# Optimization experiments

Hardware: AMD Instinct MI355X
Metric: run time of the kernel (lower is better)

The kernel has to match this reference:

```python
import jax, jax.numpy as jnp
import numpy as np

D_MODEL = 512
SEQ_LEN = 2048
S = 32  # local window size
BATCH = 2


def setup_inputs() -> dict:
    key = jax.random.key(0)
    ks = jax.random.split(key, 12)
    shp = (SEQ_LEN, BATCH, D_MODEL)
    return {
        "query": jax.random.normal(ks[0], shp, jnp.float32),
        "key": jax.random.normal(ks[1], shp, jnp.float32),
        "value": jax.random.normal(ks[2], shp, jnp.float32),
        "Wq": jax.random.normal(ks[3], (D_MODEL, D_MODEL), jnp.float32) * 0.02,
        "bq": jax.random.normal(ks[4], (D_MODEL,), jnp.float32) * 0.01,
        "Wk": jax.random.normal(ks[5], (D_MODEL, D_MODEL), jnp.float32) * 0.02,
        "bk": jax.random.normal(ks[6], (D_MODEL,), jnp.float32) * 0.01,
        "Wv": jax.random.normal(ks[7], (D_MODEL, D_MODEL), jnp.float32) * 0.02,
        "bv": jax.random.normal(ks[8], (D_MODEL,), jnp.float32) * 0.01,
        "pos_bias": jax.random.normal(ks[9], (SEQ_LEN, SEQ_LEN), jnp.float32) * 0.02,
        "Wo": jax.random.normal(ks[10], (D_MODEL, D_MODEL), jnp.float32) * 0.02,
        "bo": jax.random.normal(ks[11], (D_MODEL,), jnp.float32) * 0.01,
    }


def _aft_local(query, key, value, Wq, bq, Wk, bk, Wv, bv, pos_bias, Wo, bo):
    T, B, D = query.shape
    q = query @ Wq.T + bq  # [T,B,D]
    k = key @ Wk.T + bk
    v = value @ Wv.T + bv
    pb = pos_bias[:T, :T]

    # max_logit: elementwise max of per-dim key max and (key + col-max of pos_bias) max,
    # then batch index 0 (faithful to original `[0]` indexing) -> shape [D]
    max_logit = jnp.maximum(k.max(axis=0),
                            (k + pb.max(axis=0)[:, None, None]).max(axis=0))[0]

    # out-of-window running sums: tokens t' <= t - S contribute exp(k) (no pos bias)
    ek = jnp.exp(k - max_logit)                 # [T,B,D]
    cs_num = jnp.cumsum(ek * v, axis=0)
    cs_den = jnp.cumsum(ek, axis=0)
    t_arr = jnp.arange(T)
    prefix_idx = jnp.clip(t_arr - S, 0, T - 1)
    has_prefix = (t_arr >= S)[:, None, None]
    num_out = jnp.where(has_prefix, cs_num[prefix_idx], 0.0)
    den_out = jnp.where(has_prefix, cs_den[prefix_idx], 0.0)

    # in-window part: t' in [max(0, t-S+1), t] with pos_bias[t, t']
    j = jnp.arange(S)
    idx_raw = t_arr[:, None] - S + 1 + j[None, :]   # [T,S]
    valid = (idx_raw >= 0).astype(k.dtype)
    idx = jnp.clip(idx_raw, 0, T - 1)
    k_win = k[idx]                                  # [T,S,B,D]
    v_win = v[idx]                                  # [T,S,B,D]
    pb_win = pb[t_arr[:, None], idx]                # [T,S]
    exp_l = jnp.exp(k_win + pb_win[:, :, None, None] - max_logit) * valid[:, :, None, None]
    num_in = (exp_l * v_win).sum(axis=1)            # [T,B,D]
    den_in = exp_l.sum(axis=1)

    y = jax.nn.sigmoid(q) * (num_out + num_in) / (den_out + den_in)
    return y @ Wo.T + bo


def reference(query, key, value, Wq, bq, Wk, bk, Wv, bv, pos_bias, Wo, bo):
    return _aft_local(query, key, value, Wq, bq, Wk, bk, Wv, bv, pos_bias, Wo, bo)
```

## Files before the change

### kernel.cpp

```cpp
#include <hip/hip_runtime.h>
#include <hip/hip_bf16.h>

#define TT 2048
#define BB 2
#define DD 512
#define BD (BB*DD)
#define SS 32
#define MR (TT*BB)
#define NE (TT*BB*DD)
#define CH 32

typedef __bf16 bf16x8 __attribute__((ext_vector_type(8)));
typedef float f32x4 __attribute__((ext_vector_type(4)));

__device__ __forceinline__ void async_copy16(void* lds, const void* gptr) {
    __builtin_amdgcn_global_load_lds(
        (const __attribute__((address_space(1))) void*)gptr,
        (__attribute__((address_space(3))) void*)lds,
        16, 0, 0);
}

__global__ __launch_bounds__(256) void cast_all(
    const float* __restrict__ s0, const float* __restrict__ s1, const float* __restrict__ s2,
    const float* __restrict__ w0, const float* __restrict__ w1,
    const float* __restrict__ w2, const float* __restrict__ w3,
    __hip_bfloat16* __restrict__ d0, __hip_bfloat16* __restrict__ d1, __hip_bfloat16* __restrict__ d2,
    __hip_bfloat16* __restrict__ e0, __hip_bfloat16* __restrict__ e1,
    __hip_bfloat16* __restrict__ e2, __hip_bfloat16* __restrict__ e3)
{
    int b = blockIdx.x;
    const float* s;
    __hip_bfloat16* d;
    size_t i;
    if (b < 6144) {
        int which = b >> 11;
        s = which == 0 ? s0 : (which == 1 ? s1 : s2);
        d = which == 0 ? d0 : (which == 1 ? d1 : d2);
        i = ((size_t)(b & 2047) * 256 + threadIdx.x) * 4;
    } else {
        int b2 = b - 6144;
        int which = b2 >> 8;
        s = which == 0 ? w0 : (which == 1 ? w1 : (which == 2 ? w2 : w3));
        d = which == 0 ? e0 : (which == 1 ? e1 : (which == 2 ? e2 : e3));
        i = ((size_t)(b2 & 255) * 256 + threadIdx.x) * 4;
    }
    float4 f = *(const float4*)(s + i);
    union { __hip_bfloat16 h[4]; ushort4 u; } cv;
    cv.h[0] = __float2bfloat16(f.x); cv.h[1] = __float2bfloat16(f.y);
    cv.h[2] = __float2bfloat16(f.z); cv.h[3] = __float2bfloat16(f.w);
    *(ushort4*)((unsigned short*)d + i) = cv.u;
}

__global__ __launch_bounds__(256) void gemm_qkv(
    const __hip_bfloat16* __restrict__ qb, const __hip_bfloat16* __restrict__ kb,
    const __hip_bfloat16* __restrict__ vb,
    const __hip_bfloat16* __restrict__ Wqb, const __hip_bfloat16* __restrict__ Wkb,
    const __hip_bfloat16* __restrict__ Wvb,
    const float* __restrict__ bq, const float* __restrict__ bk,
    const float* __restrict__ bv,
    float* __restrict__ qout, float* __restrict__ ek, float* __restrict__ ekv,
    float* __restrict__ part_d, float* __restrict__ part_n)
{
    __shared__ char smem[16384];
    const int tid = threadIdx.x;
    const int lane = tid & 63;
    const int wv = tid >> 6;
    const int wave_m = wv >> 1, wave_n = wv & 1;
    const int m0 = blockIdx.y * 64, n0 = blockIdx.x * 64;
    const int kq = lane >> 4, rr = lane & 15;

    if (blockIdx.z == 0) {
        f32x4 acc[2][2] = {};
        const __hip_bfloat16* Arow = qb + (size_t)(m0 + lane) * DD + wv * 8;
        const __hip_bfloat16* Wrow = Wqb + (size_t)(n0 + lane) * DD + wv * 8;
        char* ldsA = &smem[wv * 1024];
        char* ldsW = &smem[4096 + wv * 1024];
        for (int k0 = 0; k0 < DD; k0 += 32) {
            __syncthreads();
            async_copy16(ldsA, Arow + k0);
            async_copy16(ldsW, Wrow + k0);
            __syncthreads();
            bf16x8 a0 = *(const bf16x8*)&smem[kq*1024 + (wave_m*32 +  0 + rr)*16];
            bf16x8 a1 = *(const bf16x8*)&smem[kq*1024 + (wave_m*32 + 16 + rr)*16];
            bf16x8 b0 = *(const bf16x8*)&smem[4096 + kq*1024 + (wave_n*32 +  0 + rr)*16];
            bf16x8 b1 = *(const bf16x8*)&smem[4096 + kq*1024 + (wave_n*32 + 16 + rr)*16];
            acc[0][0] = __builtin_amdgcn_mfma_f32_16x16x32_bf16(a0, b0, acc[0][0], 0, 0, 0);
            acc[0][1] = __builtin_amdgcn_mfma_f32_16x16x32_bf16(a0, b1, acc[0][1], 0, 0, 0);
            acc[1][0] = __builtin_amdgcn_mfma_f32_16x16x32_bf16(a1, b0, acc[1][0], 0, 0, 0);
            acc[1][1] = __builtin_amdgcn_mfma_f32_16x16x32_bf16(a1, b1, acc[1][1], 0, 0, 0);
        }
        #pragma unroll
        for (int ms = 0; ms < 2; ++ms)
            #pragma unroll
            for (int ns = 0; ns < 2; ++ns) {
                int n = n0 + wave_n*32 + ns*16 + rr;
                float bn = bq[n];
                #pragma unroll
                for (int r = 0; r < 4; ++r) {
                    int m = m0 + wave_m*32 + ms*16 + kq*4 + r;
                    qout[(size_t)m * DD + n] = acc[ms][ns][r] + bn;
                }
            }
    } else {
        f32x4 acck[2][2] = {}, accv[2][2] = {};
        const __hip_bfloat16* AKrow = kb + (size_t)(m0 + lane) * DD + wv * 8;
        const __hip_bfloat16* WKrow = Wkb + (size_t)(n0 + lane) * DD + wv * 8;
        const __hip_bfloat16* AVrow = vb + (size_t)(m0 + lane) * DD + wv * 8;
        const __hip_bfloat16* WVrow = Wvb + (size_t)(n0 + lane) * DD + wv * 8;
        char* ldsAK = &smem[wv * 1024];
        char* ldsWK = &smem[4096 + wv * 1024];
        char* ldsAV = &smem[8192 + wv * 1024];
        char* ldsWV = &smem[12288 + wv * 1024];
        for (int k0 = 0; k0 < DD; k0 += 32) {
            __syncthreads();
            async_copy16(ldsAK, AKrow + k0);
            async_copy16(ldsWK, WKrow + k0);
            async_copy16(ldsAV, AVrow + k0);
            async_copy16(ldsWV, WVrow + k0);
            __syncthreads();
            bf16x8 ak0 = *(const bf16x8*)&smem[kq*1024 + (wave_m*32 +  0 + rr)*16];
            bf16x8 ak1 = *(const bf16x8*)&smem[kq*1024 + (wave_m*32 + 16 + rr)*16];
            bf16x8 bk0 = *(const bf16x8*)&smem[4096 + kq*1024 + (wave_n*32 +  0 + rr)*16];
            bf16x8 bk1 = *(const bf16x8*)&smem[4096 + kq*1024 + (wave_n*32 + 16 + rr)*16];
            bf16x8 av0 = *(const bf16x8*)&smem[8192 + kq*1024 + (wave_m*32 +  0 + rr)*16];
            bf16x8 av1 = *(const bf16x8*)&smem[8192 + kq*1024 + (wave_m*32 + 16 + rr)*16];
            bf16x8 bv0 = *(const bf16x8*)&smem[12288 + kq*1024 + (wave_n*32 +  0 + rr)*16];
            bf16x8 bv1 = *(const bf16x8*)&smem[12288 + kq*1024 + (wave_n*32 + 16 + rr)*16];
            acck[0][0] = __builtin_amdgcn_mfma_f32_16x16x32_bf16(ak0, bk0, acck[0][0], 0, 0, 0);
            acck[0][1] = __builtin_amdgcn_mfma_f32_16x16x32_bf16(ak0, bk1, acck[0][1], 0, 0, 0);
            acck[1][0] = __builtin_amdgcn_mfma_f32_16x16x32_bf16(ak1, bk0, acck[1][0], 0, 0, 0);
            acck[1][1] = __builtin_amdgcn_mfma_f32_16x16x32_bf16(ak1, bk1, acck[1][1], 0, 0, 0);
            accv[0][0] = __builtin_amdgcn_mfma_f32_16x16x32_bf16(av0, bv0, accv[0][0], 0, 0, 0);
            accv[0][1] = __builtin_amdgcn_mfma_f32_16x16x32_bf16(av0, bv1, accv[0][1], 0, 0, 0);
            accv[1][0] = __builtin_amdgcn_mfma_f32_16x16x32_bf16(av1, bv0, accv[1][0], 0, 0, 0);
            accv[1][1] = __builtin_amdgcn_mfma_f32_16x16x32_bf16(av1, bv1, accv[1][1], 0, 0, 0);
        }
        float sd[2][2] = {{0.f,0.f},{0.f,0.f}};
        float sn[2][2] = {{0.f,0.f},{0.f,0.f}};
        #pragma unroll
        for (int ms = 0; ms < 2; ++ms)
            #pragma unroll
            for (int ns = 0; ns < 2; ++ns) {
                int n = n0 + wave_n*32 + ns*16 + rr;
                float bkn = bk[n], bvn = bv[n];
                #pragma unroll
                for (int r = 0; r < 4; ++r) {
                    int m = m0 + wave_m*32 + ms*16 + kq*4 + r;
                    float e  = expf(acck[ms][ns][r] + bkn);
                    float nv = e * (accv[ms][ns][r] + bvn);
                    ek[(size_t)m * DD + n]  = e;
                    ekv[(size_t)m * DD + n] = nv;
                    sd[ns][r & 1] += e;
                    sn[ns][r & 1] += nv;
                }
            }
        #pragma unroll
        for (int ns = 0; ns < 2; ++ns)
            #pragma unroll
            for (int par = 0; par < 2; ++par) {
                sd[ns][par] += __shfl_xor(sd[ns][par], 16, 64);
                sd[ns][par] += __shfl_xor(sd[ns][par], 32, 64);
                sn[ns][par] += __shfl_xor(sn[ns][par], 16, 64);
                sn[ns][par] += __shfl_xor(sn[ns][par], 32, 64);
            }
        __syncthreads();
        float* red = (float*)smem;
        if (lane < 16) {
            #pragma unroll
            for (int ns = 0; ns < 2; ++ns) {
                int c = wave_n*32 + ns*16 + rr;
                red[(0*2 + wave_m)*64 + c] = sd[ns][0];
                red[(1*2 + wave_m)*64 + c] = sd[ns][1];
                red[(2*2 + wave_m)*64 + c] = sn[ns][0];
                red[(3*2 + wave_m)*64 + c] = sn[ns][1];
            }
        }
        __syncthreads();
        {
            int which = tid >> 6;
            int c = tid & 63;
            float s = red[(which*2 + 0)*64 + c] + red[(which*2 + 1)*64 + c];
            int b = which & 1;
            float* dst = (which < 2) ? part_d : part_n;
            dst[(size_t)blockIdx.y * BD + b*512 + n0 + c] = s;
        }
    }
}

__global__ __launch_bounds__(256) void fused_window(
    const float* __restrict__ q, const float* __restrict__ ek,
    const float* __restrict__ ekv, const float* __restrict__ part_d,
    const float* __restrict__ part_n, const float* __restrict__ pb,
    __hip_bfloat16* __restrict__ yb)
{
    __shared__ float wl[CH][SS];
    const int tid = threadIdx.x;
    const int col = blockIdx.x * 256 + tid;
    const int chunk = blockIdx.y;
    const int t0 = chunk * CH;

    #pragma unroll
    for (int i = 0; i < (CH * SS) / 256; ++i) {
        int idx = tid + i * 256;
        int tl = idx >> 5, j = idx & 31;
        int t = t0 + tl;
        int u = t - (SS - 1) + j;
        float w = 0.f;
        if (u >= 0) w = expf(pb[(size_t)t * TT + u]);
        wl[tl][j] = w;
    }
    __syncthreads();

    float ring_d[32], ring_n[32];
    float cs_d = 0.f, cs_n = 0.f;
    const bool hasp = (chunk > 0);
    if (hasp) {
        float pref_d = 0.f, pref_n = 0.f;
        for (int p = 0; p < chunk; ++p) {
            pref_d += part_d[(size_t)p * BD + col];
            pref_n += part_n[(size_t)p * BD + col];
        }
        float ssd = 0.f, ssn = 0.f;
        #pragma unroll
        for (int i = 0; i < 32; ++i) {
            size_t off = (size_t)(t0 - 32 + i) * BD + col;
            float e = ek[off];
            float n = ekv[off];
            ring_d[i] = e; ring_n[i] = n;
            ssd += e; ssn += n;
        }
        cs_d = pref_d - ssd;
        cs_n = pref_n - ssn;
    } else {
        #pragma unroll
        for (int i = 0; i < 32; ++i) { ring_d[i] = 0.f; ring_n[i] = 0.f; }
    }

    #pragma unroll
    for (int s = 0; s < CH; ++s) {
        int t = t0 + s;
        size_t off = (size_t)t * BD + col;
        float e = ek[off];
        float n = ekv[off];
        cs_d += ring_d[s];
        cs_n += ring_n[s];
        ring_d[s] = e;
        ring_n[s] = n;
        float den = 0.f, num = 0.f;
        #pragma unroll
        for (int j4 = 0; j4 < 8; ++j4) {
            float4 w4 = *(const float4*)&wl[s][j4 * 4];
            den += w4.x * ring_d[(s + 1 + j4*4 + 0) & 31];
            num += w4.x * ring_n[(s + 1 + j4*4 + 0) & 31];
            den += w4.y * ring_d[(s + 1 + j4*4 + 1) & 31];
            num += w4.y * ring_n[(s + 1 + j4*4 + 1) & 31];
            den += w4.z * ring_d[(s + 1 + j4*4 + 2) & 31];
            num += w4.z * ring_n[(s + 1 + j4*4 + 2) & 31];
            den += w4.w * ring_d[(s + 1 + j4*4 + 3) & 31];
            num += w4.w * ring_n[(s + 1 + j4*4 + 3) & 31];
        }
        if (hasp) { den += cs_d; num += cs_n; }
        float qv = q[off];
        float sig = 1.f / (1.f + expf(-qv));
        yb[off] = __float2bfloat16(sig * num / den);
    }
}

__global__ __launch_bounds__(256) void gemm_out(
    const __hip_bfloat16* __restrict__ yb, const __hip_bfloat16* __restrict__ Wob,
    const float* __restrict__ bo, float* __restrict__ out)
{
    __shared__ char smem[8192];
    const int tid = threadIdx.x;
    const int lane = tid & 63;
    const int wv = tid >> 6;
    const int wave_m = wv >> 1, wave_n = wv & 1;
    const int m0 = blockIdx.y * 64, n0 = blockIdx.x * 64;
    const int kq = lane >> 4, rr = lane & 15;

    f32x4 acc[2][2] = {};
    const __hip_bfloat16* Arow = yb + (size_t)(m0 + lane) * DD + wv * 8;
    const __hip_bfloat16* Wrow = Wob + (size_t)(n0 + lane) * DD + wv * 8;
    char* ldsA = &smem[wv * 1024];
    char* ldsW = &smem[4096 + wv * 1024];

    for (int k0 = 0; k0 < DD; k0 += 32) {
        __syncthreads();
        async_copy16(ldsA, Arow + k0);
        async_copy16(ldsW, Wrow + k0);
        __syncthreads();
        bf16x8 a0 = *(const bf16x8*)&smem[kq*1024 + (wave_m*32 +  0 + rr)*16];
        bf16x8 a1 = *(const bf16x8*)&smem[kq*1024 + (wave_m*32 + 16 + rr)*16];
        bf16x8 b0 = *(const bf16x8*)&smem[4096 + kq*1024 + (wave_n*32 +  0 + rr)*16];
        bf16x8 b1 = *(const bf16x8*)&smem[4096 + kq*1024 + (wave_n*32 + 16 + rr)*16];
        acc[0][0] = __builtin_amdgcn_mfma_f32_16x16x32_bf16(a0, b0, acc[0][0], 0, 0, 0);
        acc[0][1] = __builtin_amdgcn_mfma_f32_16x16x32_bf16(a0, b1, acc[0][1], 0, 0, 0);
        acc[1][0] = __builtin_amdgcn_mfma_f32_16x16x32_bf16(a1, b0, acc[1][0], 0, 0, 0);
        acc[1][1] = __builtin_amdgcn_mfma_f32_16x16x32_bf16(a1, b1, acc[1][1], 0, 0, 0);
    }
    #pragma unroll
    for (int ms = 0; ms < 2; ++ms)
        #pragma unroll
        for (int ns = 0; ns < 2; ++ns) {
            int n = n0 + wave_n*32 + ns*16 + rr;
            float bn = bo[n];
            #pragma unroll
            for (int r = 0; r < 4; ++r) {
                int m = m0 + wave_m*32 + ms*16 + kq*4 + r;
                out[(size_t)m * DD + n] = acc[ms][ns][r] + bn;
            }
        }
}

extern "C" void kernel_launch(void* const* d_in, const int* in_sizes, int n_in,
                              void* d_out, int out_size, void* d_ws, size_t ws_size,
                              hipStream_t stream) {
    const float* query = (const float*)d_in[0];
    const float* key   = (const float*)d_in[1];
    const float* value = (const float*)d_in[2];
    const float* Wq    = (const float*)d_in[3];
    const float* bq    = (const float*)d_in[4];
    const float* Wk    = (const float*)d_in[5];
    const float* bk    = (const float*)d_in[6];
    const float* Wv    = (const float*)d_in[7];
    const float* bv    = (const float*)d_in[8];
    const float* pb    = (const float*)d_in[9];
    const float* Wo    = (const float*)d_in[10];
    const float* bo    = (const float*)d_in[11];
    float* out = (float*)d_out;

    float* ws = (float*)d_ws;
    float* q      = ws;
    float* ek     = ws + (size_t)NE;
    float* ekv    = ws + (size_t)2 * NE;
    float* part_d = ws + (size_t)3 * NE;
    float* part_n = part_d + 65536;
    __hip_bfloat16* bfb = (__hip_bfloat16*)(part_n + 65536);
    __hip_bfloat16* qb  = bfb;
    __hip_bfloat16* kb  = bfb + (size_t)NE;
    __hip_bfloat16* vb  = bfb + (size_t)2 * NE;
    __hip_bfloat16* yb  = bfb + (size_t)3 * NE;
    __hip_bfloat16* Wqb = bfb + (size_t)4 * NE;
    __hip_bfloat16* Wkb = Wqb + 262144;
    __hip_bfloat16* Wvb = Wkb + 262144;
    __hip_bfloat16* Wob = Wvb + 262144;

    cast_all<<<7168, 256, 0, stream>>>(query, key, value, Wq, Wk, Wv, Wo,
                                       qb, kb, vb, Wqb, Wkb, Wvb, Wob);

    gemm_qkv<<<dim3(DD / 64, MR / 64, 2), 256, 0, stream>>>(
        qb, kb, vb, Wqb, Wkb, Wvb, bq, bk, bv,
        q, ek, ekv, part_d, part_n);

    fused_window<<<dim3(BD / 256, TT / CH), 256, 0, stream>>>(
        q, ek, ekv, part_d, part_n, pb, yb);

    gemm_out<<<dim3(DD / 64, MR / 64), 256, 0, stream>>>(yb, Wob, bo, out);
}
```

Measured before the change: 174.9 us.

## Load MFMA fragments directly from global memory and swap GEMM grid axes

The GEMM kernels no longer stage A and W tiles through LDS with async copies and two barriers per K step. Each wave now loads its bf16x8 MFMA fragments straight from global memory, with the K loop unrolled. The grid axes are also swapped so consecutive blocks walk along M for the same N tile, which should improve L2 reuse of weight rows. This removes the barrier and LDS round trip, but wavefronts in the same block now fetch overlapping rows separately, relying on cache hits instead of shared-memory reuse.

```diff
diff --git a/kernel.cpp b/kernel.cpp
--- a/kernel.cpp
+++ b/kernel.cpp
@@ -12,13 +12,6 @@
 
 typedef __bf16 bf16x8 __attribute__((ext_vector_type(8)));
 typedef float f32x4 __attribute__((ext_vector_type(4)));
-
-__device__ __forceinline__ void async_copy16(void* lds, const void* gptr) {
-    __builtin_amdgcn_global_load_lds(
-        (const __attribute__((address_space(1))) void*)gptr,
-        (__attribute__((address_space(3))) void*)lds,
-        16, 0, 0);
-}
 
 __global__ __launch_bounds__(256) void cast_all(
     const float* __restrict__ s0, const float* __restrict__ s1, const float* __restrict__ s2,
@@ -51,6 +44,12 @@
     *(ushort4*)((unsigned short*)d + i) = cv.u;
 }
 
+__device__ __forceinline__ bf16x8 frag_ld(
+    const __hip_bfloat16* __restrict__ base, int row, int kq)
+{
+    return *(const bf16x8*)(base + (size_t)row * DD + kq * 8);
+}
+
 __global__ __launch_bounds__(256) void gemm_qkv(
     const __hip_bfloat16* __restrict__ qb, const __hip_bfloat16* __restrict__ kb,
     const __hip_bfloat16* __restrict__ vb,
@@ -61,29 +60,26 @@
     float* __restrict__ qout, float* __restrict__ ek, float* __restrict__ ekv,
     float* __restrict__ part_d, float* __restrict__ part_n)
 {
-    __shared__ char smem[16384];
+    __shared__ float red[8 * 64];
     const int tid = threadIdx.x;
     const int lane = tid & 63;
     const int wv = tid >> 6;
     const int wave_m = wv >> 1, wave_n = wv & 1;
-    const int m0 = blockIdx.y * 64, n0 = blockIdx.x * 64;
+    const int m0 = blockIdx.x * 64, n0 = blockIdx.y * 64;
     const int kq = lane >> 4, rr = lane & 15;
+    const int am0 = m0 + wave_m * 32 + rr;
+    const int bn0 = n0 + wave_n * 32 + rr;
 
     if (blockIdx.z == 0) {
         f32x4 acc[2][2] = {};
-        const __hip_bfloat16* Arow = qb + (size_t)(m0 + lane) * DD + wv * 8;
-        const __hip_bfloat16* Wrow = Wqb + (size_t)(n0 + lane) * DD + wv * 8;
-        char* ldsA = &smem[wv * 1024];
-        char* ldsW = &smem[4096 + wv * 1024];
+        #pragma unroll 8
         for (int k0 = 0; k0 < DD; k0 += 32) {
-            __syncthreads();
-            async_copy16(ldsA, Arow + k0);
-            async_copy16(ldsW, Wrow + k0);
-            __syncthreads();
-            bf16x8 a0 = *(const bf16x8*)&smem[kq*1024 + (wave_m*32 +  0 + rr)*16];
-            bf16x8 a1 = *(const bf16x8*)&smem[kq*1024 + (wave_m*32 + 16 + rr)*16];
-            bf16x8 b0 = *(const bf16x8*)&smem[4096 + kq*1024 + (wave_n*32 +  0 + rr)*16];
-            bf16x8 b1 = *(const bf16x8*)&smem[4096 + kq*1024 + (wave_n*32 + 16 + rr)*16];
+            const __hip_bfloat16* Ab = qb + k0;
+            const __hip_bfloat16* Wb = Wqb + k0;
+            bf16x8 a0 = frag_ld(Ab, am0 +  0, kq);
+            bf16x8 a1 = frag_ld(Ab, am0 + 16, kq);
+            bf16x8 b0 = frag_ld(Wb, bn0 +  0, kq);
+            bf16x8 b1 = frag_ld(Wb, bn0 + 16, kq);
             acc[0][0] = __builtin_amdgcn_mfma_f32_16x16x32_bf16(a0, b0, acc[0][0], 0, 0, 0);
             acc[0][1] = __builtin_amdgcn_mfma_f32_16x16x32_bf16(a0, b1, acc[0][1], 0, 0, 0);
             acc[1][0] = __builtin_amdgcn_mfma_f32_16x16x32_bf16(a1, b0, acc[1][0], 0, 0, 0);
@@ -103,29 +99,20 @@
             }
     } else {
         f32x4 acck[2][2] = {}, accv[2][2] = {};
-        const __hip_bfloat16* AKrow = kb + (size_t)(m0 + lane) * DD + wv * 8;
-        const __hip_bfloat16* WKrow = Wkb + (size_t)(n0 + lane) * DD + wv * 8;
-        const __hip_bfloat16* AVrow = vb + (size_t)(m0 + lane) * DD + wv * 8;
-        const __hip_bfloat16* WVrow = Wvb + (size_t)(n0 + lane) * DD + wv * 8;
-        char* ldsAK = &smem[wv * 1024];
-        char* ldsWK = &smem[4096 + wv * 1024];
-        char* ldsAV = &smem[8192 + wv * 1024];
-        char* ldsWV = &smem[12288 + wv * 1024];
+        #pragma unroll 4
         for (int k0 = 0; k0 < DD; k0 += 32) {
-            __syncthreads();
-            async_copy16(ldsAK, AKrow + k0);
-            async_copy16(ldsWK, WKrow + k0);
-            async_copy16(ldsAV, AVrow + k0);
-            async_copy16(ldsWV, WVrow + k0);
-            __syncthreads();
-            bf16x8 ak0 = *(const bf16x8*)&smem[kq*1024 + (wave_m*32 +  0 + rr)*16];
-            bf16x8 ak1 = *(const bf16x8*)&smem[kq*1024 + (wave_m*32 + 16 + rr)*16];
-            bf16x8 bk0 = *(const bf16x8*)&smem[4096 + kq*1024 + (wave_n*32 +  0 + rr)*16];
-            bf16x8 bk1 = *(const bf16x8*)&smem[4096 + kq*1024 + (wave_n*32 + 16 + rr)*16];
-            bf16x8 av0 = *(const bf16x8*)&smem[8192 + kq*1024 + (wave_m*32 +  0 + rr)*16];
-            bf16x8 av1 = *(const bf16x8*)&smem[8192 + kq*1024 + (wave_m*32 + 16 + rr)*16];
-            bf16x8 bv0 = *(const bf16x8*)&smem[12288 + kq*1024 + (wave_n*32 +  0 + rr)*16];
-            bf16x8 bv1 = *(const bf16x8*)&smem[12288 + kq*1024 + (wave_n*32 + 16 + rr)*16];
+            const __hip_bfloat16* AK = kb + k0;
+            const __hip_bfloat16* WK = Wkb + k0;
+            const __hip_bfloat16* AV = vb + k0;
+            const __hip_bfloat16* WV = Wvb + k0;
+            bf16x8 ak0 = frag_ld(AK, am0 +  0, kq);
+            bf16x8 ak1 = frag_ld(AK, am0 + 16, kq);
+            bf16x8 bk0 = frag_ld(WK, bn0 +  0, kq);
+            bf16x8 bk1 = frag_ld(WK, bn0 + 16, kq);
+            bf16x8 av0 = frag_ld(AV, am0 +  0, kq);
+            bf16x8 av1 = frag_ld(AV, am0 + 16, kq);
+            bf16x8 bv0 = frag_ld(WV, bn0 +  0, kq);
+            bf16x8 bv1 = frag_ld(WV, bn0 + 16, kq);
             acck[0][0] = __builtin_amdgcn_mfma_f32_16x16x32_bf16(ak0, bk0, acck[0][0], 0, 0, 0);
             acck[0][1] = __builtin_amdgcn_mfma_f32_16x16x32_bf16(ak0, bk1, acck[0][1], 0, 0, 0);
             acck[1][0] = __builtin_amdgcn_mfma_f32_16x16x32_bf16(ak1, bk0, acck[1][0], 0, 0, 0);
@@ -164,7 +151,6 @@
                 sn[ns][par] += __shfl_xor(sn[ns][par], 32, 64);
             }
         __syncthreads();
-        float* red = (float*)smem;
         if (lane < 16) {
             #pragma unroll
             for (int ns = 0; ns < 2; ++ns) {
@@ -182,7 +168,7 @@
             float s = red[(which*2 + 0)*64 + c] + red[(which*2 + 1)*64 + c];
             int b = which & 1;
             float* dst = (which < 2) ? part_d : part_n;
-            dst[(size_t)blockIdx.y * BD + b*512 + n0 + c] = s;
+            dst[(size_t)blockIdx.x * BD + b*512 + n0 + c] = s;
         }
     }
 }
@@ -270,29 +256,24 @@
     const __hip_bfloat16* __restrict__ yb, const __hip_bfloat16* __restrict__ Wob,
     const float* __restrict__ bo, float* __restrict__ out)
 {
-    __shared__ char smem[8192];
     const int tid = threadIdx.x;
     const int lane = tid & 63;
     const int wv = tid >> 6;
     const int wave_m = wv >> 1, wave_n = wv & 1;
-    const int m0 = blockIdx.y * 64, n0 = blockIdx.x * 64;
+    const int m0 = blockIdx.x * 64, n0 = blockIdx.y * 64;
     const int kq = lane >> 4, rr = lane & 15;
+    const int am0 = m0 + wave_m * 32 + rr;
+    const int bn0 = n0 + wave_n * 32 + rr;
 
     f32x4 acc[2][2] = {};
-    const __hip_bfloat16* Arow = yb + (size_t)(m0 + lane) * DD + wv * 8;
-    const __hip_bfloat16* Wrow = Wob + (size_t)(n0 + lane) * DD + wv * 8;
-    char* ldsA = &smem[wv * 1024];
-    char* ldsW = &smem[4096 + wv * 1024];
-
+    #pragma unroll 8
     for (int k0 = 0; k0 < DD; k0 += 32) {
-        __syncthreads();
-        async_copy16(ldsA, Arow + k0);
-        async_copy16(ldsW, Wrow + k0);
-        __syncthreads();
-        bf16x8 a0 = *(const bf16x8*)&smem[kq*1024 + (wave_m*32 +  0 + rr)*16];
-        bf16x8 a1 = *(const bf16x8*)&smem[kq*1024 + (wave_m*32 + 16 + rr)*16];
-        bf16x8 b0 = *(const bf16x8*)&smem[4096 + kq*1024 + (wave_n*32 +  0 + rr)*16];
-        bf16x8 b1 = *(const bf16x8*)&smem[4096 + kq*1024 + (wave_n*32 + 16 + rr)*16];
+        const __hip_bfloat16* Ab = yb + k0;
+        const __hip_bfloat16* Wb = Wob + k0;
+        bf16x8 a0 = frag_ld(Ab, am0 +  0, kq);
+        bf16x8 a1 = frag_ld(Ab, am0 + 16, kq);
+        bf16x8 b0 = frag_ld(Wb, bn0 +  0, kq);
+        bf16x8 b1 = frag_ld(Wb, bn0 + 16, kq);
         acc[0][0] = __builtin_amdgcn_mfma_f32_16x16x32_bf16(a0, b0, acc[0][0], 0, 0, 0);
         acc[0][1] = __builtin_amdgcn_mfma_f32_16x16x32_bf16(a0, b1, acc[0][1], 0, 0, 0);
         acc[1][0] = __builtin_amdgcn_mfma_f32_16x16x32_bf16(a1, b0, acc[1][0], 0, 0, 0);
@@ -348,12 +329,12 @@
     cast_all<<<7168, 256, 0, stream>>>(query, key, value, Wq, Wk, Wv, Wo,
                                        qb, kb, vb, Wqb, Wkb, Wvb, Wob);
 
-    gemm_qkv<<<dim3(DD / 64, MR / 64, 2), 256, 0, stream>>>(
+    gemm_qkv<<<dim3(MR / 64, DD / 64, 2), 256, 0, stream>>>(
         qb, kb, vb, Wqb, Wkb, Wvb, bq, bk, bv,
         q, ek, ekv, part_d, part_n);
 
     fused_window<<<dim3(BD / 256, TT / CH), 256, 0, stream>>>(
         q, ek, ekv, part_d, part_n, pb, yb);
 
-    gemm_out<<<dim3(DD / 64, MR / 64), 256, 0, stream>>>(yb, Wob, bo, out);
-}
+    gemm_out<<<dim3(MR / 64, DD / 64), 256, 0, stream>>>(yb, Wob, bo, out);
+}
```

Result: slower. 210.1 us (+20.2%).

## Double-buffer LDS tiles in QKV and output GEMMs to overlap loads

Applied to the files above, without the earlier changes.

The three GEMM kernels now keep two LDS tile buffers. The first tile is prefetched before the loop, and each k-step issues the async global-to-LDS copy for the next step before reading the current buffer. This drops one of the two barriers per iteration and lets global load latency overlap with the MFMA work. In exchange, LDS per block grows to 32 KB, which may limit how many blocks fit on each CU.

```diff
diff --git a/kernel.cpp b/kernel.cpp
--- a/kernel.cpp
+++ b/kernel.cpp
@@ -61,7 +61,7 @@
     float* __restrict__ qout, float* __restrict__ ek, float* __restrict__ ekv,
     float* __restrict__ part_d, float* __restrict__ part_n)
 {
-    __shared__ char smem[16384];
+    __shared__ char smem[32768];
     const int tid = threadIdx.x;
     const int lane = tid & 63;
     const int wv = tid >> 6;
@@ -73,17 +73,21 @@
         f32x4 acc[2][2] = {};
         const __hip_bfloat16* Arow = qb + (size_t)(m0 + lane) * DD + wv * 8;
         const __hip_bfloat16* Wrow = Wqb + (size_t)(n0 + lane) * DD + wv * 8;
-        char* ldsA = &smem[wv * 1024];
-        char* ldsW = &smem[4096 + wv * 1024];
+        async_copy16(&smem[wv * 1024], Arow);
+        async_copy16(&smem[4096 + wv * 1024], Wrow);
         for (int k0 = 0; k0 < DD; k0 += 32) {
             __syncthreads();
-            async_copy16(ldsA, Arow + k0);
-            async_copy16(ldsW, Wrow + k0);
-            __syncthreads();
-            bf16x8 a0 = *(const bf16x8*)&smem[kq*1024 + (wave_m*32 +  0 + rr)*16];
-            bf16x8 a1 = *(const bf16x8*)&smem[kq*1024 + (wave_m*32 + 16 + rr)*16];
-            bf16x8 b0 = *(const bf16x8*)&smem[4096 + kq*1024 + (wave_n*32 +  0 + rr)*16];
-            bf16x8 b1 = *(const bf16x8*)&smem[4096 + kq*1024 + (wave_n*32 + 16 + rr)*16];
+            const int cur = (k0 >> 5) & 1;
+            const int nxt = cur ^ 1;
+            if (k0 + 32 < DD) {
+                async_copy16(&smem[nxt * 16384 + wv * 1024], Arow + k0 + 32);
+                async_copy16(&smem[nxt * 16384 + 4096 + wv * 1024], Wrow + k0 + 32);
+            }
+            const char* base = &smem[cur * 16384];
+            bf16x8 a0 = *(const bf16x8*)&base[kq*1024 + (wave_m*32 +  0 + rr)*16];
+            bf16x8 a1 = *(const bf16x8*)&base[kq*1024 + (wave_m*32 + 16 + rr)*16];
+            bf16x8 b0 = *(const bf16x8*)&base[4096 + kq*1024 + (wave_n*32 +  0 + rr)*16];
+            bf16x8 b1 = *(const bf16x8*)&base[4096 + kq*1024 + (wave_n*32 + 16 + rr)*16];
             acc[0][0] = __builtin_amdgcn_mfma_f32_16x16x32_bf16(a0, b0, acc[0][0], 0, 0, 0);
             acc[0][1] = __builtin_amdgcn_mfma_f32_16x16x32_bf16(a0, b1, acc[0][1], 0, 0, 0);
             acc[1][0] = __builtin_amdgcn_mfma_f32_16x16x32_bf16(a1, b0, acc[1][0], 0, 0, 0);
@@ -107,25 +111,29 @@
         const __hip_bfloat16* WKrow = Wkb + (size_t)(n0 + lane) * DD + wv * 8;
         const __hip_bfloat16* AVrow = vb + (size_t)(m0 + lane) * DD + wv * 8;
         const __hip_bfloat16* WVrow = Wvb + (size_t)(n0 + lane) * DD + wv * 8;
-        char* ldsAK = &smem[wv * 1024];
-        char* ldsWK = &smem[4096 + wv * 1024];
-        char* ldsAV = &smem[8192 + wv * 1024];
-        char* ldsWV = &smem[12288 + wv * 1024];
+        async_copy16(&smem[        wv * 1024], AKrow);
+        async_copy16(&smem[ 4096 + wv * 1024], WKrow);
+        async_copy16(&smem[ 8192 + wv * 1024], AVrow);
+        async_copy16(&smem[12288 + wv * 1024], WVrow);
         for (int k0 = 0; k0 < DD; k0 += 32) {
             __syncthreads();
-            async_copy16(ldsAK, AKrow + k0);
-            async_copy16(ldsWK, WKrow + k0);
-            async_copy16(ldsAV, AVrow + k0);
-            async_copy16(ldsWV, WVrow + k0);
-            __syncthreads();
-            bf16x8 ak0 = *(const bf16x8*)&smem[kq*1024 + (wave_m*32 +  0 + rr)*16];
-            bf16x8 ak1 = *(const bf16x8*)&smem[kq*1024 + (wave_m*32 + 16 + rr)*16];
-            bf16x8 bk0 = *(const bf16x8*)&smem[4096 + kq*1024 + (wave_n*32 +  0 + rr)*16];
-            bf16x8 bk1 = *(const bf16x8*)&smem[4096 + kq*1024 + (wave_n*32 + 16 + rr)*16];
-            bf16x8 av0 = *(const bf16x8*)&smem[8192 + kq*1024 + (wave_m*32 +  0 + rr)*16];
-            bf16x8 av1 = *(const bf16x8*)&smem[8192 + kq*1024 + (wave_m*32 + 16 + rr)*16];
-            bf16x8 bv0 = *(const bf16x8*)&smem[12288 + kq*1024 + (wave_n*32 +  0 + rr)*16];
-            bf16x8 bv1 = *(const bf16x8*)&smem[12288 + kq*1024 + (wave_n*32 + 16 + rr)*16];
+            const int cur = (k0 >> 5) & 1;
+            const int nxt = cur ^ 1;
+            if (k0 + 32 < DD) {
+                async_copy16(&smem[nxt * 16384 +         wv * 1024], AKrow + k0 + 32);
+                async_copy16(&smem[nxt * 16384 +  4096 + wv * 1024], WKrow + k0 + 32);
+                async_copy16(&smem[nxt * 16384 +  8192 + wv * 1024], AVrow + k0 + 32);
+                async_copy16(&smem[nxt * 16384 + 12288 + wv * 1024], WVrow + k0 + 32);
+            }
+            const char* base = &smem[cur * 16384];
+            bf16x8 ak0 = *(const bf16x8*)&base[kq*1024 + (wave_m*32 +  0 + rr)*16];
+            bf16x8 ak1 = *(const bf16x8*)&base[kq*1024 + (wave_m*32 + 16 + rr)*16];
+            bf16x8 bk0 = *(const bf16x8*)&base[4096 + kq*1024 + (wave_n*32 +  0 + rr)*16];
+            bf16x8 bk1 = *(const bf16x8*)&base[4096 + kq*1024 + (wave_n*32 + 16 + rr)*16];
+            bf16x8 av0 = *(const bf16x8*)&base[8192 + kq*1024 + (wave_m*32 +  0 + rr)*16];
+            bf16x8 av1 = *(const bf16x8*)&base[8192 + kq*1024 + (wave_m*32 + 16 + rr)*16];
+            bf16x8 bv0 = *(const bf16x8*)&base[12288 + kq*1024 + (wave_n*32 +  0 + rr)*16];
+            bf16x8 bv1 = *(const bf16x8*)&base[12288 + kq*1024 + (wave_n*32 + 16 + rr)*16];
             acck[0][0] = __builtin_amdgcn_mfma_f32_16x16x32_bf16(ak0, bk0, acck[0][0], 0, 0, 0);
             acck[0][1] = __builtin_amdgcn_mfma_f32_16x16x32_bf16(ak0, bk1, acck[0][1], 0, 0, 0);
             acck[1][0] = __builtin_amdgcn_mfma_f32_16x16x32_bf16(ak1, bk0, acck[1][0], 0, 0, 0);
@@ -270,7 +278,7 @@
     const __hip_bfloat16* __restrict__ yb, const __hip_bfloat16* __restrict__ Wob,
     const float* __restrict__ bo, float* __restrict__ out)
 {
-    __shared__ char smem[8192];
+    __shared__ char smem[32768];
     const int tid = threadIdx.x;
     const int lane = tid & 63;
     const int wv = tid >> 6;
@@ -281,18 +289,22 @@
     f32x4 acc[2][2] = {};
     const __hip_bfloat16* Arow = yb + (size_t)(m0 + lane) * DD + wv * 8;
     const __hip_bfloat16* Wrow = Wob + (size_t)(n0 + lane) * DD + wv * 8;
-    char* ldsA = &smem[wv * 1024];
-    char* ldsW = &smem[4096 + wv * 1024];
+    async_copy16(&smem[wv * 1024], Arow);
+    async_copy16(&smem[4096 + wv * 1024], Wrow);
 
     for (int k0 = 0; k0 < DD; k0 += 32) {
         __syncthreads();
-        async_copy16(ldsA, Arow + k0);
-        async_copy16(ldsW, Wrow + k0);
-        __syncthreads();
-        bf16x8 a0 = *(const bf16x8*)&smem[kq*1024 + (wave_m*32 +  0 + rr)*16];
-        bf16x8 a1 = *(const bf16x8*)&smem[kq*1024 + (wave_m*32 + 16 + rr)*16];
-        bf16x8 b0 = *(const bf16x8*)&smem[4096 + kq*1024 + (wave_n*32 +  0 + rr)*16];
-        bf16x8 b1 = *(const bf16x8*)&smem[4096 + kq*1024 + (wave_n*32 + 16 + rr)*16];
+        const int cur = (k0 >> 5) & 1;
+        const int nxt = cur ^ 1;
+        if (k0 + 32 < DD) {
+            async_copy16(&smem[nxt * 16384 + wv * 1024], Arow + k0 + 32);
+            async_copy16(&smem[nxt * 16384 + 4096 + wv * 1024], Wrow + k0 + 32);
+        }
+        const char* base = &smem[cur * 16384];
+        bf16x8 a0 = *(const bf16x8*)&base[kq*1024 + (wave_m*32 +  0 + rr)*16];
+        bf16x8 a1 = *(const bf16x8*)&base[kq*1024 + (wave_m*32 + 16 + rr)*16];
+        bf16x8 b0 = *(const bf16x8*)&base[4096 + kq*1024 + (wave_n*32 +  0 + rr)*16];
+        bf16x8 b1 = *(const bf16x8*)&base[4096 + kq*1024 + (wave_n*32 + 16 + rr)*16];
         acc[0][0] = __builtin_amdgcn_mfma_f32_16x16x32_bf16(a0, b0, acc[0][0], 0, 0, 0);
         acc[0][1] = __builtin_amdgcn_mfma_f32_16x16x32_bf16(a0, b1, acc[0][1], 0, 0, 0);
         acc[1][0] = __builtin_amdgcn_mfma_f32_16x16x32_bf16(a1, b0, acc[1][0], 0, 0, 0);
```

After: 175.1 us. Within noise of the previous version (+0.1%).
